# Kernel tuning notes

Hardware: AMD Instinct MI355X
Metric: run time of the kernel (lower is better)

Reference implementation:

```python
import jax, jax.numpy as jnp
import numpy as np

B, S, HIDDEN = 2, 2048, 2048
HEADS, GROUPS, KVC = 16, 4, 128
HPG = HEADS // GROUPS  # heads per group
LAYER_INDEX = 2
SOFTMAX_SCALE = KVC ** -0.5
ROPE_THETA = 10000.0


def _rope_tables(seq_len, dim, dtype=jnp.float32):
    inv_freq = 1.0 / (ROPE_THETA ** (jnp.arange(0, dim, 2, dtype=jnp.float32) / dim))
    t = jnp.arange(seq_len, dtype=jnp.float32)
    freqs = jnp.outer(t, inv_freq)  # [S, dim/2]
    return jnp.cos(freqs).astype(dtype), jnp.sin(freqs).astype(dtype)


def _apply_rope(x, cos, sin):
    # x: [b, s, h, d]; rotate-half (GPT-NeoX style)
    d2 = x.shape[-1] // 2
    x1, x2 = x[..., :d2], x[..., d2:]
    c = cos[None, :, None, :]
    s = sin[None, :, None, :]
    return jnp.concatenate([x1 * c - x2 * s, x2 * c + x1 * s], axis=-1)


def setup_inputs() -> dict:
    key = jax.random.key(0)
    k1, k2, k3, k4 = jax.random.split(key, 4)
    std = HIDDEN ** -0.5
    return {
        "x": jax.random.normal(k1, (B, S, HIDDEN), dtype=jnp.float32),
        "w_q": jax.random.normal(k2, (HIDDEN, HEADS * KVC), dtype=jnp.float32) * std,
        "w_kv": jax.random.normal(k3, (HIDDEN, 2 * GROUPS * KVC), dtype=jnp.float32) * std,
        "w_dense": jax.random.normal(k4, (HEADS * KVC, HIDDEN), dtype=jnp.float32) * std,
    }


def reference(x, w_q, w_kv, w_dense):
    b, s, _ = x.shape
    # QKV projections
    q = (x @ w_q).reshape(b, s, HEADS, KVC)                 # [b,s,H,d]
    kv = (x @ w_kv).reshape(b, s, 2, GROUPS, KVC)
    k, v = kv[:, :, 0], kv[:, :, 1]                          # [b,s,G,d]
    # Rotary embeddings on q and k
    cos, sin = _rope_tables(s, KVC, x.dtype)
    q = _apply_rope(q, cos, sin)
    k = _apply_rope(k, cos, sin)
    # GQA attention with per-layer scaling trick:
    # scores computed at scale/softmax of layer_index, cast fp32, rescaled back.
    qg = q.reshape(b, s, GROUPS, HPG, KVC)
    scores = jnp.einsum("bqghd,bkgd->bghqk", qg, k) * (SOFTMAX_SCALE / LAYER_INDEX)
    scores = scores.astype(jnp.float32) * LAYER_INDEX
    # causal mask
    causal = jnp.tril(jnp.ones((s, s), dtype=bool))
    mask_value = jnp.finfo(jnp.float32).min
    scores = jnp.where(causal[None, None, None, :, :], scores, mask_value)
    probs = jax.nn.softmax(scores, axis=-1).astype(x.dtype)  # dropout p=0 (eval)
    ctx = jnp.einsum("bghqk,bkgd->bqghd", probs, v).reshape(b, s, HEADS * KVC)
    return ctx @ w_dense
```

## Files before the change

kernel.cpp:

```cpp
#include <hip/hip_runtime.h>
#include <hip/hip_bf16.h>
#include <stdint.h>

typedef unsigned short u16;
typedef __bf16 bf16x8 __attribute__((ext_vector_type(8)));
typedef float f32x4 __attribute__((ext_vector_type(4)));

#define S_LEN 2048
#define BATCH 2
#define NHEADS 16
#define NGROUPS 4
#define DHEAD 128
#define QKV_W 3072

__device__ __forceinline__ float bf2f(u16 u) {
  union { uint32_t i; float f; } v; v.i = ((uint32_t)u) << 16; return v.f;
}
__device__ __forceinline__ u16 f2bf(float f) {
  union { float f; uint32_t i; } v; v.f = f;
  uint32_t r = v.i + 0x7FFF + ((v.i >> 16) & 1);
  return (u16)(r >> 16);
}
__device__ __forceinline__ void llds16(const void* g, void* l) {
  __builtin_amdgcn_global_load_lds(
      (const __attribute__((address_space(1))) uint32_t*)g,
      (__attribute__((address_space(3))) uint32_t*)l, 16, 0, 0);
}

__device__ __forceinline__ void store_out(u16* C, long i, float v) { C[i] = f2bf(v); }
__device__ __forceinline__ void store_out(float* C, long i, float v) { C[i] = v; }

__global__ void rope_tables_k(float* __restrict__ cosT, float* __restrict__ sinT) {
  int i = blockIdx.x * 256 + threadIdx.x;
  int s = i >> 6, j = i & 63;
  float inv = exp2f(-(float)j * 0.20762050593045983f);
  float ang = (float)s * inv;
  float sv, cv;
  sincosf(ang, &sv, &cv);
  cosT[i] = cv; sinT[i] = sv;
}

__global__ void cvt_f32_bf16(const float* __restrict__ in, u16* __restrict__ out) {
  long i = ((long)blockIdx.x * 256 + threadIdx.x) * 4;
  float4 v = *(const float4*)(in + i);
  ushort4 o;
  o.x = f2bf(v.x); o.y = f2bf(v.y); o.z = f2bf(v.z); o.w = f2bf(v.w);
  *(ushort4*)(out + i) = o;
}

__global__ void transpose_f32_bf16(const float* __restrict__ in, u16* __restrict__ out,
                                   int R, int C) {
  __shared__ u16 tile[32][33];
  int c0 = blockIdx.x * 32, r0 = blockIdx.y * 32;
  int tx = threadIdx.x, ty = threadIdx.y;
  for (int i = 0; i < 32; i += 8)
    tile[ty + i][tx] = f2bf(in[(long)(r0 + ty + i) * C + c0 + tx]);
  __syncthreads();
  for (int i = 0; i < 32; i += 8)
    out[(long)(c0 + ty + i) * R + r0 + tx] = tile[tx][ty + i];
}


#define GFENCE() asm volatile("" ::: "memory")
#define MIDBAR() do { GFENCE(); __builtin_amdgcn_s_barrier(); \
    asm volatile("s_waitcnt lgkmcnt(0)" ::: "memory"); } while (0)
#define ENDBAR() do { GFENCE(); __builtin_amdgcn_s_barrier(); GFENCE(); } while (0)

__device__ __forceinline__ bf16x8 frag_ld(const __bf16* h, int wrow, int kk, int quad) {
  int b = ((wrow & 15) << 6) | (quad << 4);
  b ^= ((wrow >> 3) & 1) << 5;
  int off = ((((wrow >> 4) << 1) | kk) << 10) | b;
  return *(const bf16x8*)((const char*)h + off);
}

__device__ __forceinline__ void stage_half(const u16* __restrict__ g, int K,
                                           __bf16* lhalf, int wv, int lane) {
  int bsrc = (lane << 4) ^ (((lane >> 5) & 1) << 5);
  int r = bsrc >> 6, c = (bsrc & 63) >> 1;
  int cb = (wv & 1) << 5;
  llds16(g + (long)((wv >> 1) * 16 + r) * K + cb + c,
         lhalf + wv * 512 + lane * 8);
  llds16(g + (long)((4 + (wv >> 1)) * 16 + r) * K + cb + c,
         lhalf + 4096 + wv * 512 + lane * 8);
}

template <typename OutT>
__global__ __launch_bounds__(512) void gemm_bt8(
    const u16* __restrict__ A, const u16* __restrict__ Bt, OutT* __restrict__ C,
    int M, int N, int K) {
  __shared__ __align__(16) __bf16 lds[2][2][16384];
  const int tid = threadIdx.x;
  const int wv = tid >> 6, lane = tid & 63;
  const int quad = lane >> 4, l16 = lane & 15;
  const int wr = wv >> 2, wc = wv & 3;

  const int nwg = gridDim.x * gridDim.y;
  const int orig = blockIdx.y * gridDim.x + blockIdx.x;
  const int swz = (orig & 7) * (nwg >> 3) + (orig >> 3);
  const int bx = swz % gridDim.x, by = swz / gridDim.x;
  const int bm = by * 256, bn = bx * 256;

  const u16* Abase = A + (long)bm * K;
  const u16* Bbase = Bt + (long)bn * K;
  const int NT = K >> 6;

  f32x4 acc[8][4] = {};

  stage_half(Abase, K, &lds[0][0][0], wv, lane);
  stage_half(Abase + (long)128 * K, K, &lds[0][0][8192], wv, lane);
  stage_half(Bbase, K, &lds[0][1][0], wv, lane);
  stage_half(Bbase + (long)128 * K, K, &lds[0][1][8192], wv, lane);
  stage_half(Abase + 64, K, &lds[1][0][0], wv, lane);
  stage_half(Abase + (long)128 * K + 64, K, &lds[1][0][8192], wv, lane);
  stage_half(Bbase + 64, K, &lds[1][1][0], wv, lane);
  stage_half(Bbase + (long)128 * K + 64, K, &lds[1][1][8192], wv, lane);
  asm volatile("s_waitcnt vmcnt(8)" ::: "memory");
  __builtin_amdgcn_s_barrier();
  GFENCE();

  for (int kt = 0; kt < NT; ++kt) {
    const int buf = kt & 1;
    const __bf16* Ah = &lds[buf][0][wr * 8192];
    const __bf16* Bh = &lds[buf][1][(wc >> 1) * 8192];
    const int brow0 = (wc & 1) << 6;
    const bool pre = (kt + 2 < NT);
    bf16x8 aF[4][2], bF[4][2];

#pragma unroll
    for (int m = 0; m < 4; ++m) {
      aF[m][0] = frag_ld(Ah, m * 16 + l16, 0, quad);
      aF[m][1] = frag_ld(Ah, m * 16 + l16, 1, quad);
    }
#pragma unroll
    for (int n = 0; n < 2; ++n) {
      bF[n][0] = frag_ld(Bh, brow0 + n * 16 + l16, 0, quad);
      bF[n][1] = frag_ld(Bh, brow0 + n * 16 + l16, 1, quad);
    }
    MIDBAR();
    __builtin_amdgcn_s_setprio(1);
#pragma unroll
    for (int m = 0; m < 4; ++m)
#pragma unroll
      for (int n = 0; n < 2; ++n) {
        acc[m][n] = __builtin_amdgcn_mfma_f32_16x16x32_bf16(aF[m][0], bF[n][0], acc[m][n], 0, 0, 0);
        acc[m][n] = __builtin_amdgcn_mfma_f32_16x16x32_bf16(aF[m][1], bF[n][1], acc[m][n], 0, 0, 0);
      }
    __builtin_amdgcn_s_setprio(0);
    ENDBAR();

#pragma unroll
    for (int n = 2; n < 4; ++n) {
      bF[n][0] = frag_ld(Bh, brow0 + n * 16 + l16, 0, quad);
      bF[n][1] = frag_ld(Bh, brow0 + n * 16 + l16, 1, quad);
    }
    MIDBAR();
    __builtin_amdgcn_s_setprio(1);
#pragma unroll
    for (int m = 0; m < 4; ++m)
#pragma unroll
      for (int n = 2; n < 4; ++n) {
        acc[m][n] = __builtin_amdgcn_mfma_f32_16x16x32_bf16(aF[m][0], bF[n][0], acc[m][n], 0, 0, 0);
        acc[m][n] = __builtin_amdgcn_mfma_f32_16x16x32_bf16(aF[m][1], bF[n][1], acc[m][n], 0, 0, 0);
      }
    __builtin_amdgcn_s_setprio(0);
    ENDBAR();

#pragma unroll
    for (int m = 0; m < 4; ++m) {
      aF[m][0] = frag_ld(Ah, 64 + m * 16 + l16, 0, quad);
      aF[m][1] = frag_ld(Ah, 64 + m * 16 + l16, 1, quad);
    }
    if (pre) {
      const u16* p = Bbase + (long)(kt + 2) * 64;
      stage_half(p, K, &lds[buf][1][0], wv, lane);
      stage_half(p + (long)128 * K, K, &lds[buf][1][8192], wv, lane);
    }
    MIDBAR();
    __builtin_amdgcn_s_setprio(1);
#pragma unroll
    for (int m = 0; m < 4; ++m)
#pragma unroll
      for (int n = 2; n < 4; ++n) {
        acc[4 + m][n] = __builtin_amdgcn_mfma_f32_16x16x32_bf16(aF[m][0], bF[n][0], acc[4 + m][n], 0, 0, 0);
        acc[4 + m][n] = __builtin_amdgcn_mfma_f32_16x16x32_bf16(aF[m][1], bF[n][1], acc[4 + m][n], 0, 0, 0);
      }
    __builtin_amdgcn_s_setprio(0);
    ENDBAR();

    if (pre) {
      const u16* p = Abase + (long)(kt + 2) * 64;
      stage_half(p, K, &lds[buf][0][0], wv, lane);
      stage_half(p + (long)128 * K, K, &lds[buf][0][8192], wv, lane);
    }
    MIDBAR();
    __builtin_amdgcn_s_setprio(1);
#pragma unroll
    for (int m = 0; m < 4; ++m)
#pragma unroll
      for (int n = 0; n < 2; ++n) {
        acc[4 + m][n] = __builtin_amdgcn_mfma_f32_16x16x32_bf16(aF[m][0], bF[n][0], acc[4 + m][n], 0, 0, 0);
        acc[4 + m][n] = __builtin_amdgcn_mfma_f32_16x16x32_bf16(aF[m][1], bF[n][1], acc[4 + m][n], 0, 0, 0);
      }
    __builtin_amdgcn_s_setprio(0);
    if (pre) { asm volatile("s_waitcnt vmcnt(8)" ::: "memory"); }
    else     { asm volatile("s_waitcnt vmcnt(0)" ::: "memory"); }
    ENDBAR();
  }

  const long colbase = (long)bn + wc * 64 + l16;
#pragma unroll
  for (int mt = 0; mt < 8; ++mt)
#pragma unroll
    for (int nt = 0; nt < 4; ++nt)
#pragma unroll
      for (int rr = 0; rr < 4; ++rr) {
        long row = bm + wr * 128 + mt * 16 + quad * 4 + rr;
        store_out(C, row * N + colbase + nt * 16, acc[mt][nt][rr]);
      }
}

__global__ void rope_q_k(u16* __restrict__ qkv, const float* __restrict__ cosT,
                         const float* __restrict__ sinT) {
  long i = (long)blockIdx.x * 256 + threadIdx.x;
  int j = i & 63;
  long rest = i >> 6;
  int h = rest & 15;
  long bs = rest >> 4;
  int s = bs & (S_LEN - 1);
  long base = bs * QKV_W + h * DHEAD + j;
  float x1 = bf2f(qkv[base]), x2 = bf2f(qkv[base + 64]);
  float c = cosT[s * 64 + j], sn = sinT[s * 64 + j];
  qkv[base] = f2bf(x1 * c - x2 * sn);
  qkv[base + 64] = f2bf(x2 * c + x1 * sn);
}

__global__ void rope_k_k(const u16* __restrict__ qkv, u16* __restrict__ Kb,
                         const float* __restrict__ cosT, const float* __restrict__ sinT) {
  long i = (long)blockIdx.x * 256 + threadIdx.x;
  int j = i & 63;
  long rest = i >> 6;
  int g = rest & 3;
  long bs = rest >> 2;
  int s = bs & (S_LEN - 1);
  int b = (int)(bs >> 11);
  long src = bs * QKV_W + 2048 + g * 128 + j;
  float x1 = bf2f(qkv[src]), x2 = bf2f(qkv[src + 64]);
  float c = cosT[s * 64 + j], sn = sinT[s * 64 + j];
  long dst = ((long)(b * NGROUPS + g) * S_LEN + s) * DHEAD + j;
  Kb[dst] = f2bf(x1 * c - x2 * sn);
  Kb[dst + 64] = f2bf(x2 * c + x1 * sn);
}

__global__ void v_trans_k(const u16* __restrict__ qkv, u16* __restrict__ Vt) {
  __shared__ u16 tile[32][33];
  int s0 = blockIdx.x * 32, d0 = blockIdx.y * 32;
  int bg = blockIdx.z;
  int b = bg >> 2, g = bg & 3;
  int tx = threadIdx.x, ty = threadIdx.y;
  for (int i = 0; i < 32; i += 8) {
    long s = s0 + ty + i;
    tile[ty + i][tx] = qkv[((long)b * S_LEN + s) * QKV_W + 2560 + g * 128 + d0 + tx];
  }
  __syncthreads();
  for (int i = 0; i < 32; i += 8) {
    int d = d0 + ty + i;
    Vt[((long)(b * NGROUPS + g) * DHEAD + d) * S_LEN + s0 + tx] = tile[tx][ty + i];
  }
}

__global__ __launch_bounds__(256, 2) void attn_k5(
    const u16* __restrict__ Q,
    const u16* __restrict__ Kb,
    const u16* __restrict__ Vt,
    u16* __restrict__ ctx) {
  __shared__ __align__(16) __bf16 Ks[2][64 * 128];
  __shared__ __align__(16) __bf16 Vts[2][128 * 64];
  __shared__ __align__(16) __bf16 Ps[64 * 64];

  const int h = blockIdx.y, b = blockIdx.z, g = h >> 2;
  const int tid = threadIdx.x, wv = tid >> 6, lane = tid & 63;
  const int quad = lane >> 4, l16 = lane & 15;
  const float SCALE = 0.08838834764831845f;

  const long kbase = (long)(b * NGROUPS + g) * S_LEN * DHEAD;
  const long vbase = (long)(b * NGROUPS + g) * DHEAD * S_LEN;

  const int krow_off = lane >> 4;
  const int vrow_off = lane >> 3;

  const __bf16 oneb = (__bf16)((l16 == 0) ? 1.0f : 0.0f);
  const bf16x8 bones = {oneb, oneb, oneb, oneb, oneb, oneb, oneb, oneb};

  for (int pass = 0; pass < 2; ++pass) {
    const int tile = pass == 0 ? (int)blockIdx.x : 31 - (int)blockIdx.x;
    const int q0 = tile * 64;
    const int nch = tile + 1;

    bf16x8 aq[4];
    {
      const u16* qp = Q + (long)(b * S_LEN + q0 + wv * 16 + l16) * QKV_W + h * DHEAD + quad * 8;
#pragma unroll
      for (int ds = 0; ds < 4; ++ds)
        aq[ds] = *(const bf16x8*)(qp + ds * 32);
    }

#pragma unroll
    for (int i = 0; i < 4; ++i) {
      int r0 = wv * 16 + i * 4;
      int row = r0 + krow_off;
      int c = l16 ^ (row & 15);
      llds16(Kb + kbase + (long)row * DHEAD + c * 8, &Ks[0][r0 * 128 + lane * 8]);
    }
#pragma unroll
    for (int i = 0; i < 4; ++i) {
      int d0 = wv * 32 + i * 8;
      int row = d0 + vrow_off;
      int c = (lane & 7) ^ (row & 7);
      llds16(Vt + vbase + (long)row * S_LEN + c * 8, &Vts[0][d0 * 64 + lane * 8]);
    }
    __syncthreads();

    f32x4 Oacc[9] = {};

    for (int kc = 0; kc < nch; ++kc) {
      const int cur = kc & 1;
      if (kc + 1 < nch) {
        const int nxt = cur ^ 1;
#pragma unroll
        for (int i = 0; i < 4; ++i) {
          int r0 = wv * 16 + i * 4;
          int row = r0 + krow_off;
          int c = l16 ^ (row & 15);
          llds16(Kb + kbase + (long)((kc + 1) * 64 + row) * DHEAD + c * 8,
                 &Ks[nxt][r0 * 128 + lane * 8]);
        }
#pragma unroll
        for (int i = 0; i < 4; ++i) {
          int d0 = wv * 32 + i * 8;
          int row = d0 + vrow_off;
          int c = (lane & 7) ^ (row & 7);
          llds16(Vt + vbase + (long)row * S_LEN + (kc + 1) * 64 + c * 8,
                 &Vts[nxt][d0 * 64 + lane * 8]);
        }
      }

      f32x4 sacc[4] = {};
#pragma unroll
      for (int ds = 0; ds < 4; ++ds) {
        int pos0 = ((ds * 4 + quad) ^ l16) * 8;
#pragma unroll
        for (int nt = 0; nt < 4; ++nt) {
          bf16x8 bk = *(const bf16x8*)&Ks[cur][(nt * 16 + l16) * 128 + pos0];
          sacc[nt] = __builtin_amdgcn_mfma_f32_16x16x32_bf16(aq[ds], bk, sacc[nt], 0, 0, 0);
        }
      }

#pragma unroll
      for (int nt = 0; nt < 4; ++nt)
#pragma unroll
        for (int r = 0; r < 4; ++r) {
          int qrow = q0 + wv * 16 + quad * 4 + r;
          int key = kc * 64 + nt * 16 + l16;
          float p = (key <= qrow) ? __expf(sacc[nt][r] * SCALE) : 0.f;
          int qlocal = quad * 4 + r;
          int chunk = nt * 2 + (l16 >> 3);
          int pos = chunk ^ (qlocal & 7);
          Ps[(wv * 16 + qlocal) * 64 + pos * 8 + (l16 & 7)] = (__bf16)p;
        }

      bf16x8 ap[2];
#pragma unroll
      for (int kf = 0; kf < 2; ++kf) {
        int pos = ((kf * 4 + quad) ^ (l16 & 7)) * 8;
        ap[kf] = *(const bf16x8*)&Ps[(wv * 16 + l16) * 64 + pos];
      }
#pragma unroll
      for (int nt = 0; nt < 8; ++nt)
#pragma unroll
        for (int kf = 0; kf < 2; ++kf) {
          int pos = ((kf * 4 + quad) ^ (l16 & 7)) * 8;
          bf16x8 bv = *(const bf16x8*)&Vts[cur][(nt * 16 + l16) * 64 + pos];
          Oacc[nt] = __builtin_amdgcn_mfma_f32_16x16x32_bf16(ap[kf], bv, Oacc[nt], 0, 0, 0);
        }
      Oacc[8] = __builtin_amdgcn_mfma_f32_16x16x32_bf16(ap[0], bones, Oacc[8], 0, 0, 0);
      Oacc[8] = __builtin_amdgcn_mfma_f32_16x16x32_bf16(ap[1], bones, Oacc[8], 0, 0, 0);

      __syncthreads();
    }

    float lsum[4];
#pragma unroll
    for (int r = 0; r < 4; ++r)
      lsum[r] = __shfl(Oacc[8][r], quad << 4, 64);

    const long obase = ((long)(b * S_LEN + q0 + wv * 16) * NHEADS + h) * DHEAD;
#pragma unroll
    for (int nt = 0; nt < 8; ++nt)
#pragma unroll
      for (int r = 0; r < 4; ++r) {
        int lrow = quad * 4 + r;
        ctx[obase + (long)lrow * NHEADS * DHEAD + nt * 16 + l16] =
            f2bf(Oacc[nt][r] / lsum[r]);
      }
  }
}

extern "C" void kernel_launch(void* const* d_in, const int* in_sizes, int n_in,
                              void* d_out, int out_size, void* d_ws, size_t ws_size,
                              hipStream_t stream) {
  const float* x   = (const float*)d_in[0];
  const float* wq  = (const float*)d_in[1];
  const float* wkv = (const float*)d_in[2];
  const float* wd  = (const float*)d_in[3];
  float* out = (float*)d_out;

  char* ws = (char*)d_ws;
  float* cosT  = (float*)(ws + 0);
  float* sinT  = (float*)(ws + 524288);
  u16* wqkvT = (u16*)(ws + 1048576);
  u16* wdT   = (u16*)(ws + 13631488);
  u16* xb    = (u16*)(ws + 22020096);
  u16* qkv   = (u16*)(ws + 38797312);
  u16* Kb    = (u16*)(ws + 63963136);
  u16* Vt    = (u16*)(ws + 68157440);
  u16* ctx   = (u16*)(ws + 72351744);

  rope_tables_k<<<512, 256, 0, stream>>>(cosT, sinT);
  cvt_f32_bf16<<<8192, 256, 0, stream>>>(x, xb);
  transpose_f32_bf16<<<dim3(64, 64), dim3(32, 8), 0, stream>>>(wq, wqkvT, 2048, 2048);
  transpose_f32_bf16<<<dim3(32, 64), dim3(32, 8), 0, stream>>>(wkv, wqkvT + (long)2048 * 2048, 2048, 1024);
  transpose_f32_bf16<<<dim3(64, 64), dim3(32, 8), 0, stream>>>(wd, wdT, 2048, 2048);

  gemm_bt8<u16><<<dim3(12, 16), 512, 0, stream>>>(xb, wqkvT, qkv, 4096, 3072, 2048);

  rope_q_k<<<16384, 256, 0, stream>>>(qkv, cosT, sinT);
  rope_k_k<<<4096, 256, 0, stream>>>(qkv, Kb, cosT, sinT);
  v_trans_k<<<dim3(64, 4, 8), dim3(32, 8), 0, stream>>>(qkv, Vt);

  attn_k5<<<dim3(16, 16, 2), 256, 0, stream>>>(qkv, Kb, Vt, ctx);

  gemm_bt8<float><<<dim3(8, 16), 512, 0, stream>>>(ctx, wdT, out, 4096, 2048, 2048);
}
```

Baseline: 319.1 us.

## Widen attention query tile to 128 rows per block with mask-skip and priority hints

The attention kernel now gives each block one 128-row query tile instead of two 64-row passes. Each wave computes 32 query rows against every staged K/V chunk, so each K/V tile loaded into LDS is reused by twice as many rows. Work is balanced by reversing the tile order for batch 1 instead of pairing tiles within a block. Fully masked chunks are skipped per wave, an unmasked fast path avoids the causal compare, and s_setprio is raised around the MFMA sections. In exchange it uses more registers for the doubled accumulators and more LDS for P, which could lower occupancy.

```diff
diff --git a/kernel.cpp b/kernel.cpp
--- a/kernel.cpp
+++ b/kernel.cpp
@@ -59,7 +59,6 @@
   for (int i = 0; i < 32; i += 8)
     out[(long)(c0 + ty + i) * R + r0 + tx] = tile[tx][ty + i];
 }
-
 
 #define GFENCE() asm volatile("" ::: "memory")
 #define MIDBAR() do { GFENCE(); __builtin_amdgcn_s_barrier(); \
@@ -268,16 +267,21 @@
   }
 }
 
-__global__ __launch_bounds__(256, 2) void attn_k5(
+__global__ __launch_bounds__(256, 2) void attn_k6(
     const u16* __restrict__ Q,
     const u16* __restrict__ Kb,
     const u16* __restrict__ Vt,
     u16* __restrict__ ctx) {
   __shared__ __align__(16) __bf16 Ks[2][64 * 128];
   __shared__ __align__(16) __bf16 Vts[2][128 * 64];
-  __shared__ __align__(16) __bf16 Ps[64 * 64];
+  __shared__ __align__(16) __bf16 Ps[128 * 64];
 
   const int h = blockIdx.y, b = blockIdx.z, g = h >> 2;
+  const int tx = blockIdx.x;
+  const int tile = b ? (15 - tx) : tx;
+  const int q0 = tile * 128;
+  const int nch = 2 * (tile + 1);
+
   const int tid = threadIdx.x, wv = tid >> 6, lane = tid & 63;
   const int quad = lane >> 4, l16 = lane & 15;
   const float SCALE = 0.08838834764831845f;
@@ -291,116 +295,148 @@
   const __bf16 oneb = (__bf16)((l16 == 0) ? 1.0f : 0.0f);
   const bf16x8 bones = {oneb, oneb, oneb, oneb, oneb, oneb, oneb, oneb};
 
-  for (int pass = 0; pass < 2; ++pass) {
-    const int tile = pass == 0 ? (int)blockIdx.x : 31 - (int)blockIdx.x;
-    const int q0 = tile * 64;
-    const int nch = tile + 1;
-
-    bf16x8 aq[4];
-    {
-      const u16* qp = Q + (long)(b * S_LEN + q0 + wv * 16 + l16) * QKV_W + h * DHEAD + quad * 8;
-#pragma unroll
-      for (int ds = 0; ds < 4; ++ds)
-        aq[ds] = *(const bf16x8*)(qp + ds * 32);
-    }
-
-#pragma unroll
-    for (int i = 0; i < 4; ++i) {
-      int r0 = wv * 16 + i * 4;
-      int row = r0 + krow_off;
-      int c = l16 ^ (row & 15);
-      llds16(Kb + kbase + (long)row * DHEAD + c * 8, &Ks[0][r0 * 128 + lane * 8]);
-    }
-#pragma unroll
-    for (int i = 0; i < 4; ++i) {
-      int d0 = wv * 32 + i * 8;
-      int row = d0 + vrow_off;
-      int c = (lane & 7) ^ (row & 7);
-      llds16(Vt + vbase + (long)row * S_LEN + c * 8, &Vts[0][d0 * 64 + lane * 8]);
-    }
-    __syncthreads();
-
-    f32x4 Oacc[9] = {};
-
-    for (int kc = 0; kc < nch; ++kc) {
-      const int cur = kc & 1;
-      if (kc + 1 < nch) {
-        const int nxt = cur ^ 1;
-#pragma unroll
-        for (int i = 0; i < 4; ++i) {
-          int r0 = wv * 16 + i * 4;
-          int row = r0 + krow_off;
-          int c = l16 ^ (row & 15);
-          llds16(Kb + kbase + (long)((kc + 1) * 64 + row) * DHEAD + c * 8,
-                 &Ks[nxt][r0 * 128 + lane * 8]);
-        }
-#pragma unroll
-        for (int i = 0; i < 4; ++i) {
-          int d0 = wv * 32 + i * 8;
-          int row = d0 + vrow_off;
-          int c = (lane & 7) ^ (row & 7);
-          llds16(Vt + vbase + (long)row * S_LEN + (kc + 1) * 64 + c * 8,
-                 &Vts[nxt][d0 * 64 + lane * 8]);
-        }
-      }
-
-      f32x4 sacc[4] = {};
+  bf16x8 aq[2][4];
+#pragma unroll
+  for (int m = 0; m < 2; ++m) {
+    const u16* qp = Q + (long)(b * S_LEN + q0 + wv * 32 + m * 16 + l16) * QKV_W + h * DHEAD + quad * 8;
+#pragma unroll
+    for (int ds = 0; ds < 4; ++ds)
+      aq[m][ds] = *(const bf16x8*)(qp + ds * 32);
+  }
+
+#pragma unroll
+  for (int i = 0; i < 4; ++i) {
+    int r0 = wv * 16 + i * 4;
+    int row = r0 + krow_off;
+    int c = l16 ^ (row & 15);
+    llds16(Kb + kbase + (long)row * DHEAD + c * 8, &Ks[0][r0 * 128 + lane * 8]);
+  }
+#pragma unroll
+  for (int i = 0; i < 4; ++i) {
+    int d0 = wv * 32 + i * 8;
+    int row = d0 + vrow_off;
+    int c = (lane & 7) ^ (row & 7);
+    llds16(Vt + vbase + (long)row * S_LEN + c * 8, &Vts[0][d0 * 64 + lane * 8]);
+  }
+  __syncthreads();
+
+  f32x4 Oacc[2][8] = {};
+  f32x4 Osum[2] = {};
+  const int rmin = q0 + wv * 32;
+
+  for (int kc = 0; kc < nch; ++kc) {
+    const int cur = kc & 1;
+    if (kc + 1 < nch) {
+      const int nxt = cur ^ 1;
+#pragma unroll
+      for (int i = 0; i < 4; ++i) {
+        int r0 = wv * 16 + i * 4;
+        int row = r0 + krow_off;
+        int c = l16 ^ (row & 15);
+        llds16(Kb + kbase + (long)((kc + 1) * 64 + row) * DHEAD + c * 8,
+               &Ks[nxt][r0 * 128 + lane * 8]);
+      }
+#pragma unroll
+      for (int i = 0; i < 4; ++i) {
+        int d0 = wv * 32 + i * 8;
+        int row = d0 + vrow_off;
+        int c = (lane & 7) ^ (row & 7);
+        llds16(Vt + vbase + (long)row * S_LEN + (kc + 1) * 64 + c * 8,
+               &Vts[nxt][d0 * 64 + lane * 8]);
+      }
+    }
+
+    const bool skip = (kc * 64) > (rmin + 31);
+    if (!skip) {
+      f32x4 sacc[2][4] = {};
+      __builtin_amdgcn_s_setprio(1);
 #pragma unroll
       for (int ds = 0; ds < 4; ++ds) {
         int pos0 = ((ds * 4 + quad) ^ l16) * 8;
 #pragma unroll
         for (int nt = 0; nt < 4; ++nt) {
           bf16x8 bk = *(const bf16x8*)&Ks[cur][(nt * 16 + l16) * 128 + pos0];
-          sacc[nt] = __builtin_amdgcn_mfma_f32_16x16x32_bf16(aq[ds], bk, sacc[nt], 0, 0, 0);
+          sacc[0][nt] = __builtin_amdgcn_mfma_f32_16x16x32_bf16(aq[0][ds], bk, sacc[0][nt], 0, 0, 0);
+          sacc[1][nt] = __builtin_amdgcn_mfma_f32_16x16x32_bf16(aq[1][ds], bk, sacc[1][nt], 0, 0, 0);
         }
       }
-
-#pragma unroll
-      for (int nt = 0; nt < 4; ++nt)
-#pragma unroll
-        for (int r = 0; r < 4; ++r) {
-          int qrow = q0 + wv * 16 + quad * 4 + r;
-          int key = kc * 64 + nt * 16 + l16;
-          float p = (key <= qrow) ? __expf(sacc[nt][r] * SCALE) : 0.f;
-          int qlocal = quad * 4 + r;
-          int chunk = nt * 2 + (l16 >> 3);
-          int pos = chunk ^ (qlocal & 7);
-          Ps[(wv * 16 + qlocal) * 64 + pos * 8 + (l16 & 7)] = (__bf16)p;
+      __builtin_amdgcn_s_setprio(0);
+
+      const bool need_mask = (kc * 64 + 63) > rmin;
+      if (need_mask) {
+#pragma unroll
+        for (int m = 0; m < 2; ++m)
+#pragma unroll
+          for (int nt = 0; nt < 4; ++nt)
+#pragma unroll
+            for (int r = 0; r < 4; ++r) {
+              int qrow = rmin + m * 16 + quad * 4 + r;
+              int key = kc * 64 + nt * 16 + l16;
+              float p = (key <= qrow) ? __expf(sacc[m][nt][r] * SCALE) : 0.f;
+              int qlocal = quad * 4 + r;
+              int chunk = nt * 2 + (l16 >> 3);
+              int pos = chunk ^ (qlocal & 7);
+              Ps[(wv * 32 + m * 16 + qlocal) * 64 + pos * 8 + (l16 & 7)] = (__bf16)p;
+            }
+      } else {
+#pragma unroll
+        for (int m = 0; m < 2; ++m)
+#pragma unroll
+          for (int nt = 0; nt < 4; ++nt)
+#pragma unroll
+            for (int r = 0; r < 4; ++r) {
+              float p = __expf(sacc[m][nt][r] * SCALE);
+              int qlocal = quad * 4 + r;
+              int chunk = nt * 2 + (l16 >> 3);
+              int pos = chunk ^ (qlocal & 7);
+              Ps[(wv * 32 + m * 16 + qlocal) * 64 + pos * 8 + (l16 & 7)] = (__bf16)p;
+            }
+      }
+
+      bf16x8 ap[2][2];
+#pragma unroll
+      for (int m = 0; m < 2; ++m)
+#pragma unroll
+        for (int kf = 0; kf < 2; ++kf) {
+          int pos = ((kf * 4 + quad) ^ (l16 & 7)) * 8;
+          ap[m][kf] = *(const bf16x8*)&Ps[(wv * 32 + m * 16 + l16) * 64 + pos];
         }
-
-      bf16x8 ap[2];
-#pragma unroll
-      for (int kf = 0; kf < 2; ++kf) {
-        int pos = ((kf * 4 + quad) ^ (l16 & 7)) * 8;
-        ap[kf] = *(const bf16x8*)&Ps[(wv * 16 + l16) * 64 + pos];
-      }
+      __builtin_amdgcn_s_setprio(1);
 #pragma unroll
       for (int nt = 0; nt < 8; ++nt)
 #pragma unroll
         for (int kf = 0; kf < 2; ++kf) {
           int pos = ((kf * 4 + quad) ^ (l16 & 7)) * 8;
           bf16x8 bv = *(const bf16x8*)&Vts[cur][(nt * 16 + l16) * 64 + pos];
-          Oacc[nt] = __builtin_amdgcn_mfma_f32_16x16x32_bf16(ap[kf], bv, Oacc[nt], 0, 0, 0);
+          Oacc[0][nt] = __builtin_amdgcn_mfma_f32_16x16x32_bf16(ap[0][kf], bv, Oacc[0][nt], 0, 0, 0);
+          Oacc[1][nt] = __builtin_amdgcn_mfma_f32_16x16x32_bf16(ap[1][kf], bv, Oacc[1][nt], 0, 0, 0);
         }
-      Oacc[8] = __builtin_amdgcn_mfma_f32_16x16x32_bf16(ap[0], bones, Oacc[8], 0, 0, 0);
-      Oacc[8] = __builtin_amdgcn_mfma_f32_16x16x32_bf16(ap[1], bones, Oacc[8], 0, 0, 0);
-
-      __syncthreads();
-    }
-
+#pragma unroll
+      for (int m = 0; m < 2; ++m) {
+        Osum[m] = __builtin_amdgcn_mfma_f32_16x16x32_bf16(ap[m][0], bones, Osum[m], 0, 0, 0);
+        Osum[m] = __builtin_amdgcn_mfma_f32_16x16x32_bf16(ap[m][1], bones, Osum[m], 0, 0, 0);
+      }
+      __builtin_amdgcn_s_setprio(0);
+    }
+
+    __syncthreads();
+  }
+
+#pragma unroll
+  for (int m = 0; m < 2; ++m) {
     float lsum[4];
 #pragma unroll
     for (int r = 0; r < 4; ++r)
-      lsum[r] = __shfl(Oacc[8][r], quad << 4, 64);
-
-    const long obase = ((long)(b * S_LEN + q0 + wv * 16) * NHEADS + h) * DHEAD;
+      lsum[r] = __shfl(Osum[m][r], quad << 4, 64);
+
+    const long obase = ((long)(b * S_LEN + q0 + wv * 32 + m * 16) * NHEADS + h) * DHEAD;
 #pragma unroll
     for (int nt = 0; nt < 8; ++nt)
 #pragma unroll
       for (int r = 0; r < 4; ++r) {
         int lrow = quad * 4 + r;
         ctx[obase + (long)lrow * NHEADS * DHEAD + nt * 16 + l16] =
-            f2bf(Oacc[nt][r] / lsum[r]);
+            f2bf(Oacc[m][nt][r] / lsum[r]);
       }
   }
 }
@@ -437,7 +473,7 @@
   rope_k_k<<<4096, 256, 0, stream>>>(qkv, Kb, cosT, sinT);
   v_trans_k<<<dim3(64, 4, 8), dim3(32, 8), 0, stream>>>(qkv, Vt);
 
-  attn_k5<<<dim3(16, 16, 2), 256, 0, stream>>>(qkv, Kb, Vt, ctx);
+  attn_k6<<<dim3(16, 16, 2), 256, 0, stream>>>(qkv, Kb, Vt, ctx);
 
   gemm_bt8<float><<<dim3(8, 16), 512, 0, stream>>>(ctx, wdT, out, 4096, 2048, 2048);
 }
```

New measurement: 332.4 us. 1.04x slower.
